# Performance work log

Measured on AMD Instinct MI355X. Metric: run time of the kernel, lower is better.

The kernel has to match this reference:

```python
import jax, jax.numpy as jnp
import numpy as np


def conv3x3(x, w, b):
    # stride 1, pad 1, NCHW / OIHW
    out = jax.lax.conv_general_dilated(x, w, (1, 1), ((1, 1), (1, 1)),
                                       dimension_numbers=('NCHW', 'OIHW', 'NCHW'))
    return out + b[None, :, None, None]


def bilinear_sample(x, ys, xs):
    # x: [B,C,H,W]; ys,xs: [B,K,H,W] float sampling coords.
    # mmcv-style: zero outside image, per-corner validity.
    B, C, H, W = x.shape
    x_flat = x.reshape(B, C, H * W)
    y0 = jnp.floor(ys)
    x0 = jnp.floor(xs)
    dy = ys - y0
    dx = xs - x0
    y0i = y0.astype(jnp.int32)
    x0i = x0.astype(jnp.int32)

    def corner(yc, xc, wgt):
        valid = (yc >= 0) & (yc < H) & (xc >= 0) & (xc < W)
        idx = jnp.clip(yc, 0, H - 1) * W + jnp.clip(xc, 0, W - 1)  # [B,K,H,W]
        idx_f = idx.reshape(B, -1)
        vals = jax.vmap(lambda xf, ix: xf[:, ix])(x_flat, idx_f)  # [B,C,K*H*W]
        vals = vals.reshape(B, C, *yc.shape[1:])
        return vals * (wgt * valid)[:, None]

    out = corner(y0i, x0i, (1 - dy) * (1 - dx))
    out = out + corner(y0i, x0i + 1, (1 - dy) * dx)
    out = out + corner(y0i + 1, x0i, dy * (1 - dx))
    out = out + corner(y0i + 1, x0i + 1, dy * dx)
    return out  # [B,C,K,H,W]


def avgpool3s2(z):
    # AvgPool2d(kernel=3, stride=2, padding=1), count_include_pad=True -> divide by 9
    s = jax.lax.reduce_window(z, 0.0, jax.lax.add, (1, 1, 3, 3), (1, 1, 2, 2),
                              ((0, 0), (0, 0), (1, 1), (1, 1)))
    return s / 9.0


def setup_inputs() -> dict:
    key = jax.random.key(0)
    k1, k2, k3 = jax.random.split(key, 3)
    C = 64
    x = jax.random.normal(k1, (4, C, 128, 128), dtype=jnp.float32)
    w_off = jax.random.normal(k2, (27, C, 3, 3), dtype=jnp.float32) * 0.02
    b_off = jnp.zeros((27,), dtype=jnp.float32)
    w_align = jax.random.normal(k3, (C, C, 3, 3), dtype=jnp.float32) * 0.02
    b_align = jnp.zeros((C,), dtype=jnp.float32)
    return {"x": x, "w_off": w_off, "b_off": b_off, "w_align": w_align, "b_align": b_align}


def reference(x, w_off, b_off, w_align, b_align):
    B, C, H, W = x.shape
    K = 9
    off_all = conv3x3(x, w_off, b_off)               # [B,27,H,W]
    offset = off_all[:, :2 * K]                      # [B,18,H,W]
    mask = 2.0 * jax.nn.sigmoid(off_all[:, 2 * K:])  # [B,9,H,W]
    off = offset.reshape(B, K, 2, H, W)
    dy = off[:, :, 0]
    dx = off[:, :, 1]
    # base kernel grid (dilation 1, pad 1): offsets in {-1,0,1}
    ky = (jnp.arange(K) // 3 - 1).astype(jnp.float32)
    kx = (jnp.arange(K) % 3 - 1).astype(jnp.float32)
    ys = jnp.arange(H, dtype=jnp.float32)[None, None, :, None] + ky[None, :, None, None] + dy
    xs = jnp.arange(W, dtype=jnp.float32)[None, None, None, :] + kx[None, :, None, None] + dx
    sampled = bilinear_sample(x, ys, xs) * mask[:, None]    # [B,C,K,H,W]
    w = jnp.einsum('bckhw,ock->bohw', sampled, w_align.reshape(C, C, K))
    w = w + b_align[None, :, None, None]
    w = jnp.exp(jax.nn.sigmoid(w))
    return avgpool3s2(w * x) / avgpool3s2(w)
```

## Files before the change

### kernel.cpp

```cpp
#include <hip/hip_runtime.h>
#include <hip/hip_bf16.h>

#define HW 16384
#define CC 64
#define BB 4

typedef __attribute__((ext_vector_type(8))) short bf8;
typedef __attribute__((ext_vector_type(4))) float f4;

static __device__ __forceinline__ float bf2f(unsigned short u) {
    return __uint_as_float(((unsigned)u) << 16);
}
static __device__ __forceinline__ unsigned short f2bf(float f) {
    __hip_bfloat16 h = __float2bfloat16(f);
    return *reinterpret_cast<unsigned short*>(&h);
}

__global__ __launch_bounds__(256) void k_prep_tx(const float* __restrict__ x,
                                                 const float* __restrict__ w_off,
                                                 const float* __restrict__ w_align,
                                                 unsigned short* __restrict__ xT,
                                                 unsigned short* __restrict__ wA2,
                                                 unsigned short* __restrict__ Wal2) {
    __shared__ unsigned T32[64 * 33];
    int bx = blockIdx.x, t = threadIdx.x;
    if (bx < 216) {
        int i = bx * 256 + t;
        if (i < 32 * 576) {
            int jj = i & 7;
            int chunk = i >> 3;
            int l = chunk & 63;
            int g = chunk >> 6;
            int m2 = g & 1;
            int h2 = (g >> 1) & 1;
            int tp = g >> 2;
            int m = m2 * 16 + (l & 15);
            int c = h2 * 32 + (l >> 4) * 8 + jj;
            float v = (m < 27) ? w_off[m * 576 + c * 9 + tp] : 0.f;
            wA2[i] = f2bf(v);
        } else {
            int j = i - 32 * 576;
            int jj = j & 7;
            int chunk = j >> 3;
            int l = chunk & 63;
            int g = chunk >> 6;
            int mt = g & 3;
            int th = g >> 2;
            int h2 = th & 1;
            int tp = th >> 1;
            int o = mt * 16 + (l & 15);
            int c = h2 * 32 + (l >> 4) * 8 + jj;
            Wal2[j] = f2bf(w_align[o * 576 + c * 9 + tp]);
        }
        return;
    }
    int pix0 = (bx - 216) * 64;
    int b = pix0 >> 14, hw0 = pix0 & (HW - 1);
    const float* xb = x + (size_t)b * CC * HW + hw0;
#pragma unroll
    for (int u = 0; u < 8; u++) {
        int i = t + 256 * u;
        int cp = i >> 6, p = i & 63;
        float v0 = xb[(size_t)(2 * cp) * HW + p];
        float v1 = xb[(size_t)(2 * cp + 1) * HW + p];
        T32[p * 33 + cp] = (unsigned)f2bf(v0) | ((unsigned)f2bf(v1) << 16);
    }
    __syncthreads();
#pragma unroll
    for (int u = 0; u < 2; u++) {
        int i = t + 256 * u;
        int p = i >> 3, q = i & 7;
        uint4 qq;
        qq.x = T32[p * 33 + q * 4 + 0];
        qq.y = T32[p * 33 + q * 4 + 1];
        qq.z = T32[p * 33 + q * 4 + 2];
        qq.w = T32[p * 33 + q * 4 + 3];
        *(uint4*)(xT + ((size_t)b * HW + hw0 + p) * CC + q * 8) = qq;
    }
}

__global__ __launch_bounds__(512, 4) void k_fused(const unsigned short* __restrict__ xT,
                                                  const unsigned short* __restrict__ wA2,
                                                  const unsigned short* __restrict__ Wal2,
                                                  const float* __restrict__ b_off,
                                                  const float* __restrict__ b_align,
                                                  float* __restrict__ wten) {
    __shared__ __align__(16) unsigned short TF[420 * 64];
    __shared__ float OB[27 * 133];

    int t = threadIdx.x, lane = t & 63, wv = t >> 6;
    int quad = lane >> 4, col = lane & 15;
    int bx = blockIdx.x;
    int b = bx >> 7;
    int r = bx & 127;
    int h0 = (r >> 1) * 2;
    int w0 = (r & 1) * 64;
    int pxo = wv * 16 + col;
    int rr = pxo >> 6;
    int hp = h0 + rr, wp = w0 + (pxo & 63);
    int px = (hp << 7) + wp;
    const unsigned short* xTb = xT + (size_t)b * HW * CC;
    const unsigned short* wl = Wal2 + lane * 8;

#pragma unroll
    for (int u = 0; u < 7; u++) {
        int i = t + 512 * u;
        if (i < 3360) {
            int e = i >> 3, s = i & 7;
            int ty = e / 70, tx = e - ty * 70;
            int gy = min(max(h0 - 2 + ty, 0), 127);
            int gx = min(max(w0 - 3 + tx, 0), 127);
            int c = s ^ (e & 7);
            uint4 q = *(const uint4*)(xTb + ((size_t)((gy << 7) + gx)) * CC + c * 8);
            *(uint4*)(TF + i * 8) = q;
        }
    }
    __syncthreads();

    {
        const bf8 zero = {0, 0, 0, 0, 0, 0, 0, 0};
        f4 a0 = {0.f, 0.f, 0.f, 0.f};
        f4 a1 = {0.f, 0.f, 0.f, 0.f};
#pragma unroll
        for (int tap = 0; tap < 9; tap++) {
            int dyt = tap / 3 - 1, dxt = tap - (tap / 3) * 3 - 1;
            int hs = hp + dyt, ws = wp + dxt;
            bool valid = ((unsigned)hs < 128u) && ((unsigned)ws < 128u);
            int e = (rr + dyt + 2) * 70 + (pxo & 63) + dxt + 3;
            int sL = quad ^ (e & 7);
            bf8 b0 = *(const bf8*)(TF + e * 64 + (sL << 3));
            bf8 b1 = *(const bf8*)(TF + e * 64 + ((sL ^ 4) << 3));
            b0 = valid ? b0 : zero;
            b1 = valid ? b1 : zero;
            const bf8 a00 = *(const bf8*)(wA2 + (((tap * 4 + 0) * 64 + lane) << 3));
            const bf8 a01 = *(const bf8*)(wA2 + (((tap * 4 + 1) * 64 + lane) << 3));
            const bf8 a10 = *(const bf8*)(wA2 + (((tap * 4 + 2) * 64 + lane) << 3));
            const bf8 a11 = *(const bf8*)(wA2 + (((tap * 4 + 3) * 64 + lane) << 3));
            a0 = __builtin_amdgcn_mfma_f32_16x16x32_bf16(a00, b0, a0, 0, 0, 0);
            a1 = __builtin_amdgcn_mfma_f32_16x16x32_bf16(a01, b0, a1, 0, 0, 0);
            a0 = __builtin_amdgcn_mfma_f32_16x16x32_bf16(a10, b1, a0, 0, 0, 0);
            a1 = __builtin_amdgcn_mfma_f32_16x16x32_bf16(a11, b1, a1, 0, 0, 0);
        }
#pragma unroll
        for (int i = 0; i < 4; i++) {
            int o0 = quad * 4 + i;
            OB[o0 * 133 + pxo] = a0[i] + b_off[o0];
            int o1 = 16 + o0;
            if (o1 < 27) {
                float v = a1[i] + b_off[o1];
                if (o1 >= 18) v = 2.f / (1.f + __expf(-v));
                OB[o1 * 133 + pxo] = v;
            }
        }
    }

    float dyv[9], dxv[9], mv[9];
#pragma unroll
    for (int k = 0; k < 9; k++) {
        dyv[k] = OB[(2 * k) * 133 + pxo];
        dxv[k] = OB[(2 * k + 1) * 133 + pxo];
        mv[k]  = OB[(18 + k) * 133 + pxo];
    }

    int hm2 = h0 - 2, hp3 = h0 + 3, wm3 = w0 - 3, wp66 = w0 + 66;

    f4 acc[4];
#pragma unroll
    for (int mt = 0; mt < 4; mt++) acc[mt] = (f4){0.f, 0.f, 0.f, 0.f};

#pragma unroll
    for (int k = 0; k < 9; k++) {
        float dy = dyv[k], dx = dxv[k], m = mv[k];
        int k3 = k / 3;
        float ys = (float)(hp + k3 - 1) + dy;
        float xs = (float)(wp + (k - 3 * k3) - 1) + dx;
        float y0f = floorf(ys), x0f = floorf(xs);
        float fy = ys - y0f, fx = xs - x0f;
        int y0 = (int)y0f, x0 = (int)x0f;
        int y1 = y0 + 1, x1 = x0 + 1;
        bool vy0 = (unsigned)y0 < 128u, vy1 = (unsigned)y1 < 128u;
        bool vx0 = (unsigned)x0 < 128u, vx1 = (unsigned)x1 < 128u;
        int cy0 = min(max(y0, 0), 127), cy1 = min(max(y1, 0), 127);
        int cx0 = min(max(x0, 0), 127), cx1 = min(max(x1, 0), 127);
        float w00 = (1.f - fy) * (1.f - fx) * ((vy0 && vx0) ? m : 0.f);
        float w01 = (1.f - fy) * fx         * ((vy0 && vx1) ? m : 0.f);
        float w10 = fy * (1.f - fx)         * ((vy1 && vx0) ? m : 0.f);
        float w11 = fy * fx                 * ((vy1 && vx1) ? m : 0.f);

        bool inT = (cy0 >= hm2) & (cy1 <= hp3) & (cx0 >= wm3) & (cx1 <= wp66);
        uint4 qa0, qa1, qa2, qa3, qb0, qb1, qb2, qb3;
        if (inT) {
            int r0 = (cy0 - hm2) * 70 - wm3, r1 = (cy1 - hm2) * 70 - wm3;
            int e00 = r0 + cx0, e01 = r0 + cx1, e10 = r1 + cx0, e11 = r1 + cx1;
            int s00 = quad ^ (e00 & 7), s01 = quad ^ (e01 & 7);
            int s10 = quad ^ (e10 & 7), s11 = quad ^ (e11 & 7);
            qa0 = *(const uint4*)(TF + e00 * 64 + (s00 << 3));
            qa1 = *(const uint4*)(TF + e01 * 64 + (s01 << 3));
            qa2 = *(const uint4*)(TF + e10 * 64 + (s10 << 3));
            qa3 = *(const uint4*)(TF + e11 * 64 + (s11 << 3));
            qb0 = *(const uint4*)(TF + e00 * 64 + ((s00 ^ 4) << 3));
            qb1 = *(const uint4*)(TF + e01 * 64 + ((s01 ^ 4) << 3));
            qb2 = *(const uint4*)(TF + e10 * 64 + ((s10 ^ 4) << 3));
            qb3 = *(const uint4*)(TF + e11 * 64 + ((s11 ^ 4) << 3));
        } else {
            const unsigned short* c00 = xTb + ((size_t)(cy0 * 128 + cx0)) * CC + quad * 8;
            const unsigned short* c01 = xTb + ((size_t)(cy0 * 128 + cx1)) * CC + quad * 8;
            const unsigned short* c10 = xTb + ((size_t)(cy1 * 128 + cx0)) * CC + quad * 8;
            const unsigned short* c11 = xTb + ((size_t)(cy1 * 128 + cx1)) * CC + quad * 8;
            qa0 = *(const uint4*)(c00);      qa1 = *(const uint4*)(c01);
            qa2 = *(const uint4*)(c10);      qa3 = *(const uint4*)(c11);
            qb0 = *(const uint4*)(c00 + 32); qb1 = *(const uint4*)(c01 + 32);
            qb2 = *(const uint4*)(c10 + 32); qb3 = *(const uint4*)(c11 + 32);
        }

        bf8 bfrag[2];
#pragma unroll
        for (int h2 = 0; h2 < 2; h2++) {
            const unsigned short* u00 = (const unsigned short*)(h2 ? &qb0 : &qa0);
            const unsigned short* u01 = (const unsigned short*)(h2 ? &qb1 : &qa1);
            const unsigned short* u10 = (const unsigned short*)(h2 ? &qb2 : &qa2);
            const unsigned short* u11 = (const unsigned short*)(h2 ? &qb3 : &qa3);
            unsigned short ov[8];
#pragma unroll
            for (int j = 0; j < 8; j++) {
                float v = w00 * bf2f(u00[j]) + w01 * bf2f(u01[j])
                        + w10 * bf2f(u10[j]) + w11 * bf2f(u11[j]);
                ov[j] = f2bf(v);
            }
            bfrag[h2] = *(const bf8*)ov;
        }
#pragma unroll
        for (int h2 = 0; h2 < 2; h2++) {
#pragma unroll
            for (int mt = 0; mt < 4; mt++) {
                const bf8 a = *(const bf8*)(wl + (size_t)(((k * 2 + h2) * 4 + mt) * 512));
                acc[mt] = __builtin_amdgcn_mfma_f32_16x16x32_bf16(a, bfrag[h2], acc[mt], 0, 0, 0);
            }
        }
    }

    float* wb = wten + (size_t)b * CC * HW + px;
#pragma unroll
    for (int mt = 0; mt < 4; mt++)
#pragma unroll
        for (int i = 0; i < 4; i++) {
            int o = mt * 16 + quad * 4 + i;
            float u = acc[mt][i] + b_align[o];
            float sg = 1.f / (1.f + __expf(-u));
            wb[(size_t)o * HW] = __expf(sg);
        }
}

__global__ __launch_bounds__(256) void k_pool(const float* __restrict__ x,
                                              const float* __restrict__ wten,
                                              float* __restrict__ out) {
    int idx = blockIdx.x * 256 + threadIdx.x;
    int ow = idx & 63;
    int oh = (idx >> 6) & 63;
    int bc = idx >> 12;
    const float* wp = wten + (size_t)bc * HW;
    const float* xp = x + (size_t)bc * HW;
    float num = 0.f, den = 0.f;
#pragma unroll
    for (int iy = 0; iy < 3; iy++) {
        int y = 2 * oh + iy - 1;
        if ((unsigned)y >= 128u) continue;
#pragma unroll
        for (int ix = 0; ix < 3; ix++) {
            int xc = 2 * ow + ix - 1;
            if ((unsigned)xc >= 128u) continue;
            float wv = wp[y * 128 + xc];
            float xv = xp[y * 128 + xc];
            num = fmaf(wv, xv, num);
            den += wv;
        }
    }
    out[idx] = num / den;
}

extern "C" void kernel_launch(void* const* d_in, const int* in_sizes, int n_in,
                              void* d_out, int out_size, void* d_ws, size_t ws_size,
                              hipStream_t stream) {
    const float* x       = (const float*)d_in[0];
    const float* w_off   = (const float*)d_in[1];
    const float* b_off   = (const float*)d_in[2];
    const float* w_align = (const float*)d_in[3];
    const float* b_align = (const float*)d_in[4];
    float* out = (float*)d_out;

    char* p = (char*)d_ws;
    float* wten = (float*)p;                  p += (size_t)BB * CC * HW * 4;
    unsigned short* xT  = (unsigned short*)p; p += (size_t)BB * HW * CC * 2;
    unsigned short* wA2 = (unsigned short*)p; p += 32 * 576 * 2;
    unsigned short* Wal2 = (unsigned short*)p;

    k_prep_tx<<<dim3(1240), dim3(256), 0, stream>>>(x, w_off, w_align, xT, wA2, Wal2);
    k_fused<<<dim3(512), dim3(512), 0, stream>>>(xT, wA2, Wal2, b_off, b_align, wten);
    k_pool<<<dim3(4096), dim3(256), 0, stream>>>(x, wten, out);
}
```

Measured before the change: 110.3 us.

## Apply bilinear weights after MFMA per corner instead of interpolating inputs

Instead of interpolating the four bilinear corners into one bf16 fragment on the VALU and then running a single MFMA chain, each corner is multiplied by the weight matrix separately with MFMA. The per-pixel bilinear weights are then applied to the fp32 outputs with FMAs. This removes the bf16 unpack/convert/repack VALU work and the rounding of the interpolated value, at the cost of 4x more MFMA instructions. It also unifies the LDS/global load path with pointer selects and an XOR address trick, and lowers the launch-bounds occupancy hint from 4 to 3 to allow more registers.

```diff
diff --git a/kernel.cpp b/kernel.cpp
--- a/kernel.cpp
+++ b/kernel.cpp
@@ -8,9 +8,6 @@
 typedef __attribute__((ext_vector_type(8))) short bf8;
 typedef __attribute__((ext_vector_type(4))) float f4;
 
-static __device__ __forceinline__ float bf2f(unsigned short u) {
-    return __uint_as_float(((unsigned)u) << 16);
-}
 static __device__ __forceinline__ unsigned short f2bf(float f) {
     __hip_bfloat16 h = __float2bfloat16(f);
     return *reinterpret_cast<unsigned short*>(&h);
@@ -79,7 +76,7 @@
     }
 }
 
-__global__ __launch_bounds__(512, 4) void k_fused(const unsigned short* __restrict__ xT,
+__global__ __launch_bounds__(512, 3) void k_fused(const unsigned short* __restrict__ xT,
                                                   const unsigned short* __restrict__ wA2,
                                                   const unsigned short* __restrict__ Wal2,
                                                   const float* __restrict__ b_off,
@@ -101,6 +98,7 @@
     int px = (hp << 7) + wp;
     const unsigned short* xTb = xT + (size_t)b * HW * CC;
     const unsigned short* wl = Wal2 + lane * 8;
+    const unsigned short* TFg = TF;
 
 #pragma unroll
     for (int u = 0; u < 7; u++) {
@@ -154,14 +152,6 @@
         }
     }
 
-    float dyv[9], dxv[9], mv[9];
-#pragma unroll
-    for (int k = 0; k < 9; k++) {
-        dyv[k] = OB[(2 * k) * 133 + pxo];
-        dxv[k] = OB[(2 * k + 1) * 133 + pxo];
-        mv[k]  = OB[(18 + k) * 133 + pxo];
-    }
-
     int hm2 = h0 - 2, hp3 = h0 + 3, wm3 = w0 - 3, wp66 = w0 + 66;
 
     f4 acc[4];
@@ -169,15 +159,16 @@
     for (int mt = 0; mt < 4; mt++) acc[mt] = (f4){0.f, 0.f, 0.f, 0.f};
 
 #pragma unroll
-    for (int k = 0; k < 9; k++) {
-        float dy = dyv[k], dx = dxv[k], m = mv[k];
-        int k3 = k / 3;
+    for (int j = 0; j < 9; j++) {
+        float dy = OB[(2 * j) * 133 + pxo];
+        float dx = OB[(2 * j + 1) * 133 + pxo];
+        float m  = OB[(18 + j) * 133 + pxo];
+        const int k3 = j / 3, kx = j - 3 * k3;
         float ys = (float)(hp + k3 - 1) + dy;
-        float xs = (float)(wp + (k - 3 * k3) - 1) + dx;
+        float xs = (float)(wp + kx - 1) + dx;
         float y0f = floorf(ys), x0f = floorf(xs);
         float fy = ys - y0f, fx = xs - x0f;
-        int y0 = (int)y0f, x0 = (int)x0f;
-        int y1 = y0 + 1, x1 = x0 + 1;
+        int y0 = (int)y0f, x0 = (int)x0f, y1 = y0 + 1, x1 = x0 + 1;
         bool vy0 = (unsigned)y0 < 128u, vy1 = (unsigned)y1 < 128u;
         bool vx0 = (unsigned)x0 < 128u, vx1 = (unsigned)x1 < 128u;
         int cy0 = min(max(y0, 0), 127), cy1 = min(max(y1, 0), 127);
@@ -188,53 +179,46 @@
         float w11 = fy * fx                 * ((vy1 && vx1) ? m : 0.f);
 
         bool inT = (cy0 >= hm2) & (cy1 <= hp3) & (cx0 >= wm3) & (cx1 <= wp66);
-        uint4 qa0, qa1, qa2, qa3, qb0, qb1, qb2, qb3;
-        if (inT) {
-            int r0 = (cy0 - hm2) * 70 - wm3, r1 = (cy1 - hm2) * 70 - wm3;
-            int e00 = r0 + cx0, e01 = r0 + cx1, e10 = r1 + cx0, e11 = r1 + cx1;
-            int s00 = quad ^ (e00 & 7), s01 = quad ^ (e01 & 7);
-            int s10 = quad ^ (e10 & 7), s11 = quad ^ (e11 & 7);
-            qa0 = *(const uint4*)(TF + e00 * 64 + (s00 << 3));
-            qa1 = *(const uint4*)(TF + e01 * 64 + (s01 << 3));
-            qa2 = *(const uint4*)(TF + e10 * 64 + (s10 << 3));
-            qa3 = *(const uint4*)(TF + e11 * 64 + (s11 << 3));
-            qb0 = *(const uint4*)(TF + e00 * 64 + ((s00 ^ 4) << 3));
-            qb1 = *(const uint4*)(TF + e01 * 64 + ((s01 ^ 4) << 3));
-            qb2 = *(const uint4*)(TF + e10 * 64 + ((s10 ^ 4) << 3));
-            qb3 = *(const uint4*)(TF + e11 * 64 + ((s11 ^ 4) << 3));
-        } else {
-            const unsigned short* c00 = xTb + ((size_t)(cy0 * 128 + cx0)) * CC + quad * 8;
-            const unsigned short* c01 = xTb + ((size_t)(cy0 * 128 + cx1)) * CC + quad * 8;
-            const unsigned short* c10 = xTb + ((size_t)(cy1 * 128 + cx0)) * CC + quad * 8;
-            const unsigned short* c11 = xTb + ((size_t)(cy1 * 128 + cx1)) * CC + quad * 8;
-            qa0 = *(const uint4*)(c00);      qa1 = *(const uint4*)(c01);
-            qa2 = *(const uint4*)(c10);      qa3 = *(const uint4*)(c11);
-            qb0 = *(const uint4*)(c00 + 32); qb1 = *(const uint4*)(c01 + 32);
-            qb2 = *(const uint4*)(c10 + 32); qb3 = *(const uint4*)(c11 + 32);
-        }
-
-        bf8 bfrag[2];
-#pragma unroll
-        for (int h2 = 0; h2 < 2; h2++) {
-            const unsigned short* u00 = (const unsigned short*)(h2 ? &qb0 : &qa0);
-            const unsigned short* u01 = (const unsigned short*)(h2 ? &qb1 : &qa1);
-            const unsigned short* u10 = (const unsigned short*)(h2 ? &qb2 : &qa2);
-            const unsigned short* u11 = (const unsigned short*)(h2 ? &qb3 : &qa3);
-            unsigned short ov[8];
-#pragma unroll
-            for (int j = 0; j < 8; j++) {
-                float v = w00 * bf2f(u00[j]) + w01 * bf2f(u01[j])
-                        + w10 * bf2f(u10[j]) + w11 * bf2f(u11[j]);
-                ov[j] = f2bf(v);
-            }
-            bfrag[h2] = *(const bf8*)ov;
-        }
-#pragma unroll
-        for (int h2 = 0; h2 < 2; h2++) {
-#pragma unroll
-            for (int mt = 0; mt < 4; mt++) {
-                const bf8 a = *(const bf8*)(wl + (size_t)(((k * 2 + h2) * 4 + mt) * 512));
-                acc[mt] = __builtin_amdgcn_mfma_f32_16x16x32_bf16(a, bfrag[h2], acc[mt], 0, 0, 0);
+        int r0 = (cy0 - hm2) * 70 - wm3, r1 = (cy1 - hm2) * 70 - wm3;
+        int e00 = r0 + cx0, e01 = r0 + cx1, e10 = r1 + cx0, e11 = r1 + cx1;
+        const unsigned short* p00 = inT ? (TFg + e00 * 64 + ((quad ^ (e00 & 7)) << 3))
+            : xTb + ((size_t)((cy0 << 7) + cx0)) * CC + quad * 8;
+        const unsigned short* p01 = inT ? (TFg + e01 * 64 + ((quad ^ (e01 & 7)) << 3))
+            : xTb + ((size_t)((cy0 << 7) + cx1)) * CC + quad * 8;
+        const unsigned short* p10 = inT ? (TFg + e10 * 64 + ((quad ^ (e10 & 7)) << 3))
+            : xTb + ((size_t)((cy1 << 7) + cx0)) * CC + quad * 8;
+        const unsigned short* p11 = inT ? (TFg + e11 * 64 + ((quad ^ (e11 & 7)) << 3))
+            : xTb + ((size_t)((cy1 << 7) + cx1)) * CC + quad * 8;
+        bf8 q0 = *(const bf8*)p00;
+        bf8 q1 = *(const bf8*)p01;
+        bf8 q2 = *(const bf8*)p10;
+        bf8 q3 = *(const bf8*)p11;
+        bf8 q4 = *(const bf8*)((unsigned long long)p00 ^ 64ull);
+        bf8 q5 = *(const bf8*)((unsigned long long)p01 ^ 64ull);
+        bf8 q6 = *(const bf8*)((unsigned long long)p10 ^ 64ull);
+        bf8 q7 = *(const bf8*)((unsigned long long)p11 ^ 64ull);
+
+        const f4 z = {0.f, 0.f, 0.f, 0.f};
+#pragma unroll
+        for (int mt = 0; mt < 4; mt++) {
+            const bf8 ah0 = *(const bf8*)(wl + (size_t)(((j * 2 + 0) * 4 + mt) * 512));
+            const bf8 ah1 = *(const bf8*)(wl + (size_t)(((j * 2 + 1) * 4 + mt) * 512));
+            f4 t0 = __builtin_amdgcn_mfma_f32_16x16x32_bf16(ah0, q0, z, 0, 0, 0);
+            t0    = __builtin_amdgcn_mfma_f32_16x16x32_bf16(ah1, q4, t0, 0, 0, 0);
+            f4 t1 = __builtin_amdgcn_mfma_f32_16x16x32_bf16(ah0, q1, z, 0, 0, 0);
+            t1    = __builtin_amdgcn_mfma_f32_16x16x32_bf16(ah1, q5, t1, 0, 0, 0);
+            f4 t2 = __builtin_amdgcn_mfma_f32_16x16x32_bf16(ah0, q2, z, 0, 0, 0);
+            t2    = __builtin_amdgcn_mfma_f32_16x16x32_bf16(ah1, q6, t2, 0, 0, 0);
+            f4 t3 = __builtin_amdgcn_mfma_f32_16x16x32_bf16(ah0, q3, z, 0, 0, 0);
+            t3    = __builtin_amdgcn_mfma_f32_16x16x32_bf16(ah1, q7, t3, 0, 0, 0);
+#pragma unroll
+            for (int i = 0; i < 4; i++) {
+                float s = acc[mt][i];
+                s = fmaf(w00, t0[i], s);
+                s = fmaf(w01, t1[i], s);
+                s = fmaf(w10, t2[i], s);
+                s = fmaf(w11, t3[i], s);
+                acc[mt][i] = s;
             }
         }
     }
```

New measurement: 352.0 us. +219.3%, slower.
